# Kernel optimization log

Measured on AMD Instinct MI355X. Metric: run time of the kernel, lower is better.

## Reference

```python
import jax, jax.numpy as jnp
import numpy as np

FP8_E4M3_MAX = 448.0
BLOCK_SIZE = 128


def _block_quant_dequant_e4m3(x, block_size=BLOCK_SIZE):
    """Per-block (along last dim) FP8 E4M3 fake quantize: returns dequantized fp32."""
    M, K = x.shape
    nb = K // block_size
    xb = x.reshape(M, nb, block_size)
    amax = jnp.clip(jnp.max(jnp.abs(xb), axis=-1, keepdims=True), 1e-12, None)
    scale = FP8_E4M3_MAX / amax  # per-block scale, [M, nb, 1]
    q = jnp.clip(xb * scale, -FP8_E4M3_MAX, FP8_E4M3_MAX).astype(jnp.float8_e4m3fn)
    deq = q.astype(jnp.float32) / scale
    return deq.reshape(M, K)


def _dual_quantize_weight(w, block_size=BLOCK_SIZE):
    """TCFP-12 dual quantization: FP8 hi component + FP8-quantized residual (lo)."""
    w_hi = _block_quant_dequant_e4m3(w, block_size)
    residual = w - w_hi
    w_lo = _block_quant_dequant_e4m3(residual, block_size)
    return w_hi + w_lo


def setup_inputs() -> dict:
    key = jax.random.key(0)
    k1, k2, k3 = jax.random.split(key, 3)
    B, T, DIN, DOUT = 8, 4096, 1024, 1024
    x = jax.random.normal(k1, (B, T, DIN), dtype=jnp.float32)
    weight = jax.random.normal(k2, (DOUT, DIN), dtype=jnp.float32) * 0.02
    bias = jax.random.normal(k3, (DOUT,), dtype=jnp.float32) * 0.01
    return {"x": x, "weight": weight, "bias": bias}


def reference(x, weight, bias):
    # Block-quantize activations (fake-quant, per 128-col block, E4M3)
    B, T, DIN = x.shape
    x2d = x.reshape(-1, DIN)
    x_q = _block_quant_dequant_e4m3(x2d, BLOCK_SIZE)
    # Dual-quantize weight: hi + residual lo components
    w_q = _dual_quantize_weight(weight, BLOCK_SIZE)
    # Block-scaled GEMM (dequantized reference math) + bias
    out2d = x_q @ w_q.T + bias
    return out2d.reshape(B, T, -1)
```

## Files before the change

kernel.cpp:

```cpp
#include <hip/hip_runtime.h>
#include <hip/hip_bf16.h>

typedef __bf16 bf16x8 __attribute__((ext_vector_type(8)));
typedef float  f32x4  __attribute__((ext_vector_type(4)));

#define GLOAD_LDS16(gptr, lptr)                                                  \
  __builtin_amdgcn_global_load_lds(                                              \
      (const __attribute__((address_space(1))) void*)(gptr),                     \
      (__attribute__((address_space(3))) void*)(lptr), 16, 0, 0)

__device__ __forceinline__ unsigned short f2bf(float f) {
  __hip_bfloat16 h = __float2bfloat16(f);
  return __builtin_bit_cast(unsigned short, h);
}

__device__ __forceinline__ float groupmax32(float v) {
  v = fmaxf(v, __shfl_xor(v, 1));
  v = fmaxf(v, __shfl_xor(v, 2));
  v = fmaxf(v, __shfl_xor(v, 4));
  v = fmaxf(v, __shfl_xor(v, 8));
  v = fmaxf(v, __shfl_xor(v, 16));
  return v;
}

__device__ __forceinline__ void fq_e4m3_4(const float* __restrict__ in,
                                          float* __restrict__ out) {
  float am = fmaxf(fmaxf(fabsf(in[0]), fabsf(in[1])),
                   fmaxf(fabsf(in[2]), fabsf(in[3])));
  am = groupmax32(am);
  am = fmaxf(am, 1e-12f);
  const float scale = 448.0f / am;
  float c0 = fminf(fmaxf(in[0] * scale, -448.0f), 448.0f);
  float c1 = fminf(fmaxf(in[1] * scale, -448.0f), 448.0f);
  float c2 = fminf(fmaxf(in[2] * scale, -448.0f), 448.0f);
  float c3 = fminf(fmaxf(in[3] * scale, -448.0f), 448.0f);
  int pk = __builtin_amdgcn_cvt_pk_fp8_f32(c0, c1, 0, false);
  pk = __builtin_amdgcn_cvt_pk_fp8_f32(c2, c3, pk, true);
  out[0] = __builtin_amdgcn_cvt_f32_fp8(pk, 0) / scale;
  out[1] = __builtin_amdgcn_cvt_f32_fp8(pk, 1) / scale;
  out[2] = __builtin_amdgcn_cvt_f32_fp8(pk, 2) / scale;
  out[3] = __builtin_amdgcn_cvt_f32_fp8(pk, 3) / scale;
}

__global__ __launch_bounds__(256) void quant_x_k(const float* __restrict__ x,
                                                 unsigned short* __restrict__ xq) {
  const size_t row = blockIdx.x;
  const int tid = threadIdx.x;
  const float4 v = ((const float4*)(x + row * 1024))[tid];
  float in[4] = {v.x, v.y, v.z, v.w};
  float dq[4];
  fq_e4m3_4(in, dq);
  union { ushort4 u; unsigned short s[4]; } pk;
  pk.s[0] = f2bf(dq[0]); pk.s[1] = f2bf(dq[1]);
  pk.s[2] = f2bf(dq[2]); pk.s[3] = f2bf(dq[3]);
  ((ushort4*)(xq + row * 1024))[tid] = pk.u;
}

__global__ __launch_bounds__(256) void quant_w_k(const float* __restrict__ w,
                                                 unsigned short* __restrict__ wq) {
  const size_t row = blockIdx.x;
  const int tid = threadIdx.x;
  const float4 v = ((const float4*)(w + row * 1024))[tid];
  float in[4] = {v.x, v.y, v.z, v.w};
  float hi[4], res[4], lo[4];
  fq_e4m3_4(in, hi);
#pragma unroll
  for (int i = 0; i < 4; ++i) res[i] = in[i] - hi[i];
  fq_e4m3_4(res, lo);
  union { ushort4 u; unsigned short s[4]; } pk;
#pragma unroll
  for (int i = 0; i < 4; ++i) pk.s[i] = f2bf(hi[i] + lo[i]);
  ((ushort4*)(wq + row * 1024))[tid] = pk.u;
}

#define BM 128
#define BN 128
#define BK 64

__global__ __launch_bounds__(256) void gemm_bt_bias(
    const unsigned short* __restrict__ A,
    const unsigned short* __restrict__ B,
    const float* __restrict__ bias,
    float* __restrict__ C,
    int M, int N, int K) {
  __shared__ unsigned short ldsA[BM * BK];
  __shared__ unsigned short ldsB[BN * BK];

  const int tid  = threadIdx.x;
  const int wave = tid >> 6;
  const int lane = tid & 63;
  const int ntn  = N / BN;
  const int bn   = blockIdx.x % ntn;
  const int bm   = blockIdx.x / ntn;
  const int wr   = wave >> 1;
  const int wc   = wave & 1;

  f32x4 acc[4][4] = {};

  const int rload = wave * 32 + (lane >> 3);
  const int cload = (lane & 7) * 8;
  const unsigned short* gA = A + (size_t)(bm * BM + rload) * K + cload;
  const unsigned short* gB = B + (size_t)(bn * BN + rload) * K + cload;
  unsigned short* lA = ldsA + wave * 2048 + lane * 8;
  unsigned short* lB = ldsB + wave * 2048 + lane * 8;

  for (int kt = 0; kt < K; kt += BK) {
    __syncthreads();
#pragma unroll
    for (int t = 0; t < 4; ++t) {
      GLOAD_LDS16(gA + (size_t)(t * 8) * K + kt, lA + t * 512);
      GLOAD_LDS16(gB + (size_t)(t * 8) * K + kt, lB + t * 512);
    }
    __syncthreads();

#pragma unroll
    for (int kc = 0; kc < 2; ++kc) {
      const int kOff = kc * 32 + (lane >> 4) * 8;
      const int fRow = lane & 15;
      bf16x8 af[4], bfr[4];
#pragma unroll
      for (int i = 0; i < 4; ++i)
        af[i] = *(const bf16x8*)&ldsA[(wr * 64 + i * 16 + fRow) * BK + kOff];
#pragma unroll
      for (int j = 0; j < 4; ++j)
        bfr[j] = *(const bf16x8*)&ldsB[(wc * 64 + j * 16 + fRow) * BK + kOff];
#pragma unroll
      for (int i = 0; i < 4; ++i)
#pragma unroll
        for (int j = 0; j < 4; ++j)
          acc[i][j] = __builtin_amdgcn_mfma_f32_16x16x32_bf16(af[i], bfr[j],
                                                              acc[i][j], 0, 0, 0);
    }
  }

  const int    n0 = bn * BN + wc * 64 + (lane & 15);
  const size_t m0 = (size_t)bm * BM + wr * 64 + ((lane >> 4) << 2);
#pragma unroll
  for (int j = 0; j < 4; ++j) {
    const int col = n0 + j * 16;
    const float bv = bias[col];
#pragma unroll
    for (int i = 0; i < 4; ++i) {
      const size_t base = (m0 + (size_t)i * 16) * N + col;
#pragma unroll
      for (int r = 0; r < 4; ++r)
        C[base + (size_t)r * N] = acc[i][j][r] + bv;
    }
  }
}

extern "C" void kernel_launch(void* const* d_in, const int* in_sizes, int n_in,
                              void* d_out, int out_size, void* d_ws, size_t ws_size,
                              hipStream_t stream) {
  const float* x    = (const float*)d_in[0];
  const float* w    = (const float*)d_in[1];
  const float* bias = (const float*)d_in[2];

  const int DOUT = in_sizes[2];
  const int DIN  = in_sizes[1] / DOUT;
  const int M    = in_sizes[0] / DIN;

  unsigned short* xq = (unsigned short*)d_ws;
  unsigned short* wq = xq + (size_t)M * DIN;

  hipLaunchKernelGGL(quant_x_k, dim3(M), dim3(256), 0, stream, x, xq);
  hipLaunchKernelGGL(quant_w_k, dim3(DOUT), dim3(256), 0, stream, w, wq);

  const int grid = (M / BM) * (DOUT / BN);
  hipLaunchKernelGGL(gemm_bt_bias, dim3(grid), dim3(256), 0, stream,
                     xq, wq, bias, (float*)d_out, M, DOUT, DIN);
}
```

Before: 329.7 us.

## Swizzle GEMM LDS layout, remap blocks per XCD, batch rows in quant kernels

Applies an XOR swizzle to the 16-byte column chunks when loading A/B tiles into LDS and when reading MFMA fragments, to reduce LDS bank conflicts. Remaps GEMM block indices so each XCD works on a contiguous band of M tiles, improving L2 reuse of A and B. The quant kernels now process several rows per block to cut launch and scheduling overhead, and the per-element dequant division becomes a multiply by a precomputed reciprocal, which may differ from the reference in the last bit.

```diff
diff --git a/kernel.cpp b/kernel.cpp
--- a/kernel.cpp
+++ b/kernel.cpp
@@ -30,47 +30,58 @@
   am = groupmax32(am);
   am = fmaxf(am, 1e-12f);
   const float scale = 448.0f / am;
+  const float inv   = am * (1.0f / 448.0f);
   float c0 = fminf(fmaxf(in[0] * scale, -448.0f), 448.0f);
   float c1 = fminf(fmaxf(in[1] * scale, -448.0f), 448.0f);
   float c2 = fminf(fmaxf(in[2] * scale, -448.0f), 448.0f);
   float c3 = fminf(fmaxf(in[3] * scale, -448.0f), 448.0f);
   int pk = __builtin_amdgcn_cvt_pk_fp8_f32(c0, c1, 0, false);
   pk = __builtin_amdgcn_cvt_pk_fp8_f32(c2, c3, pk, true);
-  out[0] = __builtin_amdgcn_cvt_f32_fp8(pk, 0) / scale;
-  out[1] = __builtin_amdgcn_cvt_f32_fp8(pk, 1) / scale;
-  out[2] = __builtin_amdgcn_cvt_f32_fp8(pk, 2) / scale;
-  out[3] = __builtin_amdgcn_cvt_f32_fp8(pk, 3) / scale;
+  out[0] = __builtin_amdgcn_cvt_f32_fp8(pk, 0) * inv;
+  out[1] = __builtin_amdgcn_cvt_f32_fp8(pk, 1) * inv;
+  out[2] = __builtin_amdgcn_cvt_f32_fp8(pk, 2) * inv;
+  out[3] = __builtin_amdgcn_cvt_f32_fp8(pk, 3) * inv;
 }
 
+#define XROWS 16
 __global__ __launch_bounds__(256) void quant_x_k(const float* __restrict__ x,
                                                  unsigned short* __restrict__ xq) {
-  const size_t row = blockIdx.x;
   const int tid = threadIdx.x;
-  const float4 v = ((const float4*)(x + row * 1024))[tid];
-  float in[4] = {v.x, v.y, v.z, v.w};
-  float dq[4];
-  fq_e4m3_4(in, dq);
-  union { ushort4 u; unsigned short s[4]; } pk;
-  pk.s[0] = f2bf(dq[0]); pk.s[1] = f2bf(dq[1]);
-  pk.s[2] = f2bf(dq[2]); pk.s[3] = f2bf(dq[3]);
-  ((ushort4*)(xq + row * 1024))[tid] = pk.u;
+  const size_t row0 = (size_t)blockIdx.x * XROWS;
+#pragma unroll 4
+  for (int j = 0; j < XROWS; ++j) {
+    const size_t row = row0 + j;
+    const float4 v = ((const float4*)(x + row * 1024))[tid];
+    float in[4] = {v.x, v.y, v.z, v.w};
+    float dq[4];
+    fq_e4m3_4(in, dq);
+    union { ushort4 u; unsigned short s[4]; } pk;
+    pk.s[0] = f2bf(dq[0]); pk.s[1] = f2bf(dq[1]);
+    pk.s[2] = f2bf(dq[2]); pk.s[3] = f2bf(dq[3]);
+    ((ushort4*)(xq + row * 1024))[tid] = pk.u;
+  }
 }
 
+#define WROWS 4
 __global__ __launch_bounds__(256) void quant_w_k(const float* __restrict__ w,
                                                  unsigned short* __restrict__ wq) {
-  const size_t row = blockIdx.x;
   const int tid = threadIdx.x;
-  const float4 v = ((const float4*)(w + row * 1024))[tid];
-  float in[4] = {v.x, v.y, v.z, v.w};
-  float hi[4], res[4], lo[4];
-  fq_e4m3_4(in, hi);
+  const size_t row0 = (size_t)blockIdx.x * WROWS;
 #pragma unroll
-  for (int i = 0; i < 4; ++i) res[i] = in[i] - hi[i];
-  fq_e4m3_4(res, lo);
-  union { ushort4 u; unsigned short s[4]; } pk;
+  for (int j = 0; j < WROWS; ++j) {
+    const size_t row = row0 + j;
+    const float4 v = ((const float4*)(w + row * 1024))[tid];
+    float in[4] = {v.x, v.y, v.z, v.w};
+    float hi[4], res[4], lo[4];
+    fq_e4m3_4(in, hi);
 #pragma unroll
-  for (int i = 0; i < 4; ++i) pk.s[i] = f2bf(hi[i] + lo[i]);
-  ((ushort4*)(wq + row * 1024))[tid] = pk.u;
+    for (int i = 0; i < 4; ++i) res[i] = in[i] - hi[i];
+    fq_e4m3_4(res, lo);
+    union { ushort4 u; unsigned short s[4]; } pk;
+#pragma unroll
+    for (int i = 0; i < 4; ++i) pk.s[i] = f2bf(hi[i] + lo[i]);
+    ((ushort4*)(wq + row * 1024))[tid] = pk.u;
+  }
 }
 
 #define BM 128
@@ -89,16 +100,27 @@
   const int tid  = threadIdx.x;
   const int wave = tid >> 6;
   const int lane = tid & 63;
-  const int ntn  = N / BN;
-  const int bn   = blockIdx.x % ntn;
-  const int bm   = blockIdx.x / ntn;
-  const int wr   = wave >> 1;
-  const int wc   = wave & 1;
+  const int nbn  = N / BN;
+  const int nbm  = M / BM;
+
+  int bm, bn;
+  if ((nbm & 7) == 0) {
+    const int xcd = blockIdx.x & 7;
+    const int j   = blockIdx.x >> 3;
+    bn = j % nbn;
+    bm = xcd * (nbm >> 3) + j / nbn;
+  } else {
+    bn = blockIdx.x % nbn;
+    bm = blockIdx.x / nbn;
+  }
+
+  const int wr = wave >> 1;
+  const int wc = wave & 1;
 
   f32x4 acc[4][4] = {};
 
   const int rload = wave * 32 + (lane >> 3);
-  const int cload = (lane & 7) * 8;
+  const int cload = (((lane & 7) ^ (lane >> 3)) * 8);
   const unsigned short* gA = A + (size_t)(bm * BM + rload) * K + cload;
   const unsigned short* gB = B + (size_t)(bn * BN + rload) * K + cload;
   unsigned short* lA = ldsA + wave * 2048 + lane * 8;
@@ -113,17 +135,19 @@
     }
     __syncthreads();
 
+    const int fRow = lane & 15;
+    const int sw   = fRow & 7;
 #pragma unroll
     for (int kc = 0; kc < 2; ++kc) {
-      const int kOff = kc * 32 + (lane >> 4) * 8;
-      const int fRow = lane & 15;
+      const int c = kc * 4 + (lane >> 4);
+      const int sOff = ((c ^ sw) * 8);
       bf16x8 af[4], bfr[4];
 #pragma unroll
       for (int i = 0; i < 4; ++i)
-        af[i] = *(const bf16x8*)&ldsA[(wr * 64 + i * 16 + fRow) * BK + kOff];
+        af[i] = *(const bf16x8*)&ldsA[(wr * 64 + i * 16 + fRow) * BK + sOff];
 #pragma unroll
       for (int j = 0; j < 4; ++j)
-        bfr[j] = *(const bf16x8*)&ldsB[(wc * 64 + j * 16 + fRow) * BK + kOff];
+        bfr[j] = *(const bf16x8*)&ldsB[(wc * 64 + j * 16 + fRow) * BK + sOff];
 #pragma unroll
       for (int i = 0; i < 4; ++i)
 #pragma unroll
@@ -163,8 +187,8 @@
   unsigned short* xq = (unsigned short*)d_ws;
   unsigned short* wq = xq + (size_t)M * DIN;
 
-  hipLaunchKernelGGL(quant_x_k, dim3(M), dim3(256), 0, stream, x, xq);
-  hipLaunchKernelGGL(quant_w_k, dim3(DOUT), dim3(256), 0, stream, w, wq);
+  hipLaunchKernelGGL(quant_x_k, dim3(M / XROWS), dim3(256), 0, stream, x, xq);
+  hipLaunchKernelGGL(quant_w_k, dim3(DOUT / WROWS), dim3(256), 0, stream, w, wq);
 
   const int grid = (M / BM) * (DOUT / BN);
   hipLaunchKernelGGL(gemm_bt_bias, dim3(grid), dim3(256), 0, stream,
```

New measurement: 328.6 us. Within noise of the previous version (-0.3%).
